# Kernel optimization log

Measured on AMD Instinct MI355X. Metric: run time of the kernel, lower is better.

The kernel has to match this reference:

```python
import jax, jax.numpy as jnp
import numpy as np
from jax import lax

EPS = 1e-6

def setup_inputs() -> dict:
    key = jax.random.key(0)
    B, C, K, T = 32, 1, 128, 8000
    x = jax.random.uniform(key, (B, C, K, T), dtype=jnp.float32)
    # parameters exactly as in PCENLayer.__init__ (log of init values)
    log_s = jnp.full((1, 1, K), np.log(0.025), dtype=jnp.float32)
    log_alpha = jnp.full((1, 1, K, 1), np.log(0.8), dtype=jnp.float32)
    log_delta = jnp.full((1, 1, K, 1), np.log(10.0), dtype=jnp.float32)
    log_r = jnp.full((1, 1, K, 1), np.log(0.25), dtype=jnp.float32)
    return {"x": x, "log_s": log_s, "log_alpha": log_alpha,
            "log_delta": log_delta, "log_r": log_r}

def reference(x, log_s, log_alpha, log_delta, log_r):
    # x: [B, C, K, T]
    s = jax.nn.sigmoid(log_s)            # (1, 1, K) smoother coefficient
    init = x[..., 0]                     # init smoother from first frame

    def step(prev, xt):
        f = (1.0 - s) * prev + s * xt
        return f, f

    xs = jnp.moveaxis(x[..., 1:], -1, 0)             # (T-1, B, C, K)
    _, fs = lax.scan(step, init, xs)                 # (T-1, B, C, K)
    filtered = jnp.concatenate([init[None], fs], 0)  # (T, B, C, K)
    filtered = jnp.moveaxis(filtered, 0, -1)         # (B, C, K, T)

    alpha = jnp.exp(log_alpha)           # (1, 1, K, 1)
    delta = jnp.exp(log_delta)
    r = jnp.exp(log_r)
    return (x / (EPS + filtered) ** alpha + delta) ** r - delta ** r
```

## Files before the change

### kernel.cpp

```cpp
#include <hip/hip_runtime.h>
#include <math.h>


constexpr int   T_LEN = 8000;
constexpr int   CHUNK = 16;
constexpr int   NTH   = 512;
constexpr int   NWAVE = NTH / 64;
constexpr int   NACT  = T_LEN / CHUNK;
constexpr int   KDIM  = 128;
constexpr float EPS_F = 1e-6f;
constexpr float LOG2E = 1.4426950408889634f;

typedef float f32x4 __attribute__((ext_vector_type(4)));

__global__ __launch_bounds__(NTH, 8) void pcen_kernel(
    const float* __restrict__ x,
    const float* __restrict__ log_s,
    const float* __restrict__ log_alpha,
    const float* __restrict__ log_delta,
    const float* __restrict__ log_r,
    float* __restrict__ out)
{
    __shared__ float wAs[NWAVE], wBs[NWAVE];

    const int seq  = blockIdx.x;
    const int k    = seq & (KDIM - 1);
    const int tid  = threadIdx.x;
    const int lane = tid & 63;
    const int wave = tid >> 6;

    const float ls      = log_s[k];
    const float e_ns    = __builtin_amdgcn_exp2f(-ls * LOG2E);
    const float inv_s   = 1.0f + e_ns;
    const float s       = 1.0f / inv_s;
    const float a       = e_ns * s;
    const float alpha   = __builtin_amdgcn_exp2f(log_alpha[k] * LOG2E);
    const float delta   = __builtin_amdgcn_exp2f(log_delta[k] * LOG2E);
    const float r       = __builtin_amdgcn_exp2f(log_r[k] * LOG2E);
    const float delta_r = __builtin_amdgcn_exp2f(r * log_delta[k] * LOG2E);

    const float* xp = x   + (size_t)seq * T_LEN + tid * CHUNK;
    float*       op = out + (size_t)seq * T_LEN + tid * CHUNK;
    const bool active = tid < NACT;

    float xv[CHUNK];
    if (active) {
        #pragma unroll
        for (int v = 0; v < CHUNK / 4; ++v) {
            f32x4 t = ((const f32x4*)xp)[v];
            xv[4*v+0] = t[0]; xv[4*v+1] = t[1];
            xv[4*v+2] = t[2]; xv[4*v+3] = t[3];
        }
    }

    float A = 1.0f, B = 0.0f;
    if (active) {
        float g;
        if (tid == 0) {
            g = xv[0] * inv_s;
            #pragma unroll
            for (int j = 1; j < CHUNK; ++j) g = fmaf(a, g, xv[j]);
            A = 0.0f;
        } else {
            g = 0.0f;
            #pragma unroll
            for (int j = 0; j < CHUNK; ++j) g = fmaf(a, g, xv[j]);
            const float a2 = a * a, a4 = a2 * a2, a8 = a4 * a4;
            A = a8 * a8;
        }
        B = g;
    }

    #pragma unroll
    for (int off = 1; off < 64; off <<= 1) {
        const float pA = __shfl_up(A, off, 64);
        const float pB = __shfl_up(B, off, 64);
        if (lane >= off) {
            B = fmaf(A, pB, B);
            A = A * pA;
        }
    }

    if (lane == 63) { wAs[wave] = A; wBs[wave] = B; }
    __syncthreads();
    if (wave == 0) {
        float cA = (lane < NWAVE) ? wAs[lane] : 1.0f;
        float cB = (lane < NWAVE) ? wBs[lane] : 0.0f;
        #pragma unroll
        for (int off = 1; off < NWAVE; off <<= 1) {
            const float pA = __shfl_up(cA, off, 64);
            const float pB = __shfl_up(cB, off, 64);
            if (lane >= off) {
                cB = fmaf(cA, pB, cB);
                cA = cA * pA;
            }
        }
        if (lane < NWAVE - 1) { wAs[lane + 1] = cA; wBs[lane + 1] = cB; }
        if (lane == 0)        { wAs[0] = 1.0f;      wBs[0] = 0.0f;      }
    }
    __syncthreads();

    float eA = __shfl_up(A, 1, 64);
    float eB = __shfl_up(B, 1, 64);
    if (lane == 0) { eA = 1.0f; eB = 0.0f; }
    float fin = fmaf(eA, wBs[wave], eB);

    if (active) {
        float g = fin;
        #pragma unroll
        for (int j = 0; j < CHUNK; ++j) {
            if (j == 0 && tid == 0) g = xv[0] * inv_s;
            else                    g = fmaf(a, g, xv[j]);
            const float lg  = __builtin_amdgcn_logf(fmaf(s, g, EPS_F));
            const float inv = __builtin_amdgcn_exp2f(-alpha * lg);
            const float u   = fmaf(xv[j], inv, delta);
            xv[j] = __builtin_amdgcn_exp2f(r * __builtin_amdgcn_logf(u)) - delta_r;
        }
        #pragma unroll
        for (int v = 0; v < CHUNK / 4; ++v) {
            f32x4 t;
            t[0] = xv[4*v+0]; t[1] = xv[4*v+1];
            t[2] = xv[4*v+2]; t[3] = xv[4*v+3];
            ((f32x4*)op)[v] = t;
        }
    }
}

extern "C" void kernel_launch(void* const* d_in, const int* in_sizes, int n_in,
                              void* d_out, int out_size, void* d_ws, size_t ws_size,
                              hipStream_t stream) {
    const float* x         = (const float*)d_in[0];
    const float* log_s     = (const float*)d_in[1];
    const float* log_alpha = (const float*)d_in[2];
    const float* log_delta = (const float*)d_in[3];
    const float* log_r     = (const float*)d_in[4];
    float* out = (float*)d_out;

    const int nseq = in_sizes[0] / T_LEN;
    pcen_kernel<<<nseq, NTH, 0, stream>>>(x, log_s, log_alpha, log_delta, log_r, out);
}
```

Measured before the change: 240.7 us.

## Process four sequences per block with register prefetch of next sequence

```diff
diff --git a/kernel.cpp b/kernel.cpp
--- a/kernel.cpp
+++ b/kernel.cpp
@@ -8,6 +8,7 @@
 constexpr int   NWAVE = NTH / 64;
 constexpr int   NACT  = T_LEN / CHUNK;
 constexpr int   KDIM  = 128;
+constexpr int   GSEQ  = 4;
 constexpr float EPS_F = 1e-6f;
 constexpr float LOG2E = 1.4426950408889634f;
 
@@ -21,107 +22,113 @@
     const float* __restrict__ log_r,
     float* __restrict__ out)
 {
-    __shared__ float wAs[NWAVE], wBs[NWAVE];
+    __shared__ float wAs[2][NWAVE], wBs[2][NWAVE];
 
-    const int seq  = blockIdx.x;
-    const int k    = seq & (KDIM - 1);
     const int tid  = threadIdx.x;
     const int lane = tid & 63;
     const int wave = tid >> 6;
+    const bool active = tid < NACT;
+    const int seq0 = blockIdx.x * GSEQ;
 
-    const float ls      = log_s[k];
-    const float e_ns    = __builtin_amdgcn_exp2f(-ls * LOG2E);
-    const float inv_s   = 1.0f + e_ns;
-    const float s       = 1.0f / inv_s;
-    const float a       = e_ns * s;
-    const float alpha   = __builtin_amdgcn_exp2f(log_alpha[k] * LOG2E);
-    const float delta   = __builtin_amdgcn_exp2f(log_delta[k] * LOG2E);
-    const float r       = __builtin_amdgcn_exp2f(log_r[k] * LOG2E);
-    const float delta_r = __builtin_amdgcn_exp2f(r * log_delta[k] * LOG2E);
+    f32x4 xv[CHUNK / 4], xn[CHUNK / 4];
 
-    const float* xp = x   + (size_t)seq * T_LEN + tid * CHUNK;
-    float*       op = out + (size_t)seq * T_LEN + tid * CHUNK;
-    const bool active = tid < NACT;
-
-    float xv[CHUNK];
     if (active) {
+        const f32x4* xp = (const f32x4*)(x + (size_t)seq0 * T_LEN) + tid * (CHUNK / 4);
         #pragma unroll
-        for (int v = 0; v < CHUNK / 4; ++v) {
-            f32x4 t = ((const f32x4*)xp)[v];
-            xv[4*v+0] = t[0]; xv[4*v+1] = t[1];
-            xv[4*v+2] = t[2]; xv[4*v+3] = t[3];
-        }
-    }
-
-    float A = 1.0f, B = 0.0f;
-    if (active) {
-        float g;
-        if (tid == 0) {
-            g = xv[0] * inv_s;
-            #pragma unroll
-            for (int j = 1; j < CHUNK; ++j) g = fmaf(a, g, xv[j]);
-            A = 0.0f;
-        } else {
-            g = 0.0f;
-            #pragma unroll
-            for (int j = 0; j < CHUNK; ++j) g = fmaf(a, g, xv[j]);
-            const float a2 = a * a, a4 = a2 * a2, a8 = a4 * a4;
-            A = a8 * a8;
-        }
-        B = g;
+        for (int v = 0; v < CHUNK / 4; ++v) xv[v] = xp[v];
     }
 
     #pragma unroll
-    for (int off = 1; off < 64; off <<= 1) {
-        const float pA = __shfl_up(A, off, 64);
-        const float pB = __shfl_up(B, off, 64);
-        if (lane >= off) {
-            B = fmaf(A, pB, B);
-            A = A * pA;
+    for (int i = 0; i < GSEQ; ++i) {
+        const int seq = seq0 + i;
+        const int k   = seq & (KDIM - 1);
+        const int p   = i & 1;
+
+        if (i + 1 < GSEQ && active) {
+            const f32x4* xpn = (const f32x4*)(x + (size_t)(seq + 1) * T_LEN) + tid * (CHUNK / 4);
+            #pragma unroll
+            for (int v = 0; v < CHUNK / 4; ++v) xn[v] = xpn[v];
         }
-    }
 
-    if (lane == 63) { wAs[wave] = A; wBs[wave] = B; }
-    __syncthreads();
-    if (wave == 0) {
-        float cA = (lane < NWAVE) ? wAs[lane] : 1.0f;
-        float cB = (lane < NWAVE) ? wBs[lane] : 0.0f;
+        const float ls      = log_s[k];
+        const float e_ns    = __builtin_amdgcn_exp2f(-ls * LOG2E);
+        const float inv_s   = 1.0f + e_ns;
+        const float s       = __builtin_amdgcn_rcpf(inv_s);
+        const float a       = e_ns * s;
+        const float alpha   = __builtin_amdgcn_exp2f(log_alpha[k] * LOG2E);
+        const float delta   = __builtin_amdgcn_exp2f(log_delta[k] * LOG2E);
+        const float r       = __builtin_amdgcn_exp2f(log_r[k] * LOG2E);
+        const float delta_r = __builtin_amdgcn_exp2f(r * log_delta[k] * LOG2E);
+
+        float A = 1.0f, B = 0.0f;
+        if (active) {
+            float g;
+            if (tid == 0) {
+                g = xv[0][0] * inv_s;
+                #pragma unroll
+                for (int j = 1; j < CHUNK; ++j) g = fmaf(a, g, xv[j >> 2][j & 3]);
+                A = 0.0f;
+            } else {
+                g = 0.0f;
+                #pragma unroll
+                for (int j = 0; j < CHUNK; ++j) g = fmaf(a, g, xv[j >> 2][j & 3]);
+                const float a2 = a * a, a4 = a2 * a2, a8 = a4 * a4;
+                A = a8 * a8;
+            }
+            B = g;
+        }
+
+        #pragma unroll
+        for (int off = 1; off < 64; off <<= 1) {
+            const float pA = __shfl_up(A, off, 64);
+            const float pB = __shfl_up(B, off, 64);
+            if (lane >= off) { B = fmaf(A, pB, B); A = A * pA; }
+        }
+
+        if (lane == 63) { wAs[p][wave] = A; wBs[p][wave] = B; }
+        asm volatile("s_waitcnt lgkmcnt(0)" ::: "memory");
+        __builtin_amdgcn_s_barrier();
+
+        float cA = 1.0f, cB = 0.0f;
+        if (lane < NWAVE) { cA = wAs[p][lane]; cB = wBs[p][lane]; }
         #pragma unroll
         for (int off = 1; off < NWAVE; off <<= 1) {
             const float pA = __shfl_up(cA, off, 64);
             const float pB = __shfl_up(cB, off, 64);
-            if (lane >= off) {
-                cB = fmaf(cA, pB, cB);
-                cA = cA * pA;
+            if (lane >= off) { cB = fmaf(cA, pB, cB); cA = cA * pA; }
+        }
+        const float vin_w = __shfl(cB, wave - 1, 64);
+        const float vin   = (wave == 0) ? 0.0f : vin_w;
+
+        float eA = __shfl_up(A, 1, 64);
+        float eB = __shfl_up(B, 1, 64);
+        if (lane == 0) { eA = 1.0f; eB = 0.0f; }
+        float fin = fmaf(eA, vin, eB);
+
+        if (active) {
+            f32x4* op4 = (f32x4*)(out + (size_t)seq * T_LEN) + tid * (CHUNK / 4);
+            float g = fin;
+            #pragma unroll
+            for (int v = 0; v < CHUNK / 4; ++v) {
+                f32x4 ov;
+                #pragma unroll
+                for (int e = 0; e < 4; ++e) {
+                    const int   j  = 4 * v + e;
+                    const float xj = xv[v][e];
+                    if (j == 0 && tid == 0) g = xj * inv_s;
+                    else                    g = fmaf(a, g, xj);
+                    const float lg  = __builtin_amdgcn_logf(fmaf(s, g, EPS_F));
+                    const float inv = __builtin_amdgcn_exp2f(-alpha * lg);
+                    const float u   = fmaf(xj, inv, delta);
+                    ov[e] = __builtin_amdgcn_exp2f(r * __builtin_amdgcn_logf(u)) - delta_r;
+                }
+                op4[v] = ov;
             }
         }
-        if (lane < NWAVE - 1) { wAs[lane + 1] = cA; wBs[lane + 1] = cB; }
-        if (lane == 0)        { wAs[0] = 1.0f;      wBs[0] = 0.0f;      }
-    }
-    __syncthreads();
 
-    float eA = __shfl_up(A, 1, 64);
-    float eB = __shfl_up(B, 1, 64);
-    if (lane == 0) { eA = 1.0f; eB = 0.0f; }
-    float fin = fmaf(eA, wBs[wave], eB);
-
-    if (active) {
-        float g = fin;
-        #pragma unroll
-        for (int j = 0; j < CHUNK; ++j) {
-            if (j == 0 && tid == 0) g = xv[0] * inv_s;
-            else                    g = fmaf(a, g, xv[j]);
-            const float lg  = __builtin_amdgcn_logf(fmaf(s, g, EPS_F));
-            const float inv = __builtin_amdgcn_exp2f(-alpha * lg);
-            const float u   = fmaf(xv[j], inv, delta);
-            xv[j] = __builtin_amdgcn_exp2f(r * __builtin_amdgcn_logf(u)) - delta_r;
-        }
-        #pragma unroll
-        for (int v = 0; v < CHUNK / 4; ++v) {
-            f32x4 t;
-            t[0] = xv[4*v+0]; t[1] = xv[4*v+1];
-            t[2] = xv[4*v+2]; t[3] = xv[4*v+3];
-            ((f32x4*)op)[v] = t;
+        if (i + 1 < GSEQ) {
+            #pragma unroll
+            for (int v = 0; v < CHUNK / 4; ++v) xv[v] = xn[v];
         }
     }
 }
@@ -136,6 +143,7 @@
     const float* log_r     = (const float*)d_in[4];
     float* out = (float*)d_out;
 
-    const int nseq = in_sizes[0] / T_LEN;
-    pcen_kernel<<<nseq, NTH, 0, stream>>>(x, log_s, log_alpha, log_delta, log_r, out);
+    const int nseq    = in_sizes[0] / T_LEN;
+    const int nblocks = nseq / GSEQ;
+    pcen_kernel<<<nblocks, NTH, 0, stream>>>(x, log_s, log_alpha, log_delta, log_r, out);
 }
```

Result: slower. 247.2 us (+2.7%).
